# Kernel optimization log

Measured on AMD Instinct MI355X. Metric: run time of the kernel, lower is better.

## Reference

```python
import jax, jax.numpy as jnp
import numpy as np

K = 0.1            # manifold curvature param: points satisfy <x,x>_L = -1/K
H = 8              # num_heads
DH = 64            # head_spatial_dim
SP = 512           # spatial_dim = H*DH
SCALE = 1.0 / np.sqrt(DH)
SQRT_K = np.sqrt(K).astype(np.float32)


def _lorentz_fc(x, W, b):
    # Manifold-constrained FC: linear map to spatial coords, time recomputed
    sp = x @ W + b                                            # [..., out_spatial]
    t = jnp.sqrt(jnp.clip(1.0 / K + jnp.sum(sp * sp, axis=-1, keepdims=True), 1e-9, None))
    return jnp.concatenate([t, sp], axis=-1)


def _logmap0(p):
    # Lorentz log map at origin -> tangent spatial coords (time comp = 0)
    t, sp = p[..., :1], p[..., 1:]
    nrm = jnp.sqrt(jnp.sum(sp * sp, axis=-1, keepdims=True))
    theta = jnp.arccosh(jnp.clip(SQRT_K * t, 1.0 + 1e-7, None))
    return (theta / SQRT_K) * sp / jnp.maximum(nrm, 1e-9)


def _expmap0(u):
    nrm = jnp.sqrt(jnp.sum(u * u, axis=-1, keepdims=True))
    t = jnp.cosh(SQRT_K * nrm) / SQRT_K
    sp = jnp.sinh(SQRT_K * nrm) * u / (SQRT_K * jnp.maximum(nrm, 1e-9))
    return jnp.concatenate([t, sp], axis=-1)


def setup_inputs() -> dict:
    key = jax.random.key(0)
    ks = jax.random.split(key, 9)
    B, N = 4, 2048
    space = jax.random.normal(ks[0], (B, N, SP), dtype=jnp.float32) * 0.5
    t = jnp.sqrt(1.0 / K + jnp.sum(space * space, axis=-1, keepdims=True))
    x = jnp.concatenate([t, space], axis=-1)                  # on-manifold [B,N,513]
    s = (1 + SP) ** -0.5
    Wq = jax.random.normal(ks[1], (1 + SP, SP), dtype=jnp.float32) * s
    Wk = jax.random.normal(ks[2], (1 + SP, SP), dtype=jnp.float32) * s
    Wv = jax.random.normal(ks[3], (1 + SP, SP), dtype=jnp.float32) * s
    Wo = jax.random.normal(ks[4], (1 + SP, SP), dtype=jnp.float32) * s
    bq = jax.random.normal(ks[5], (SP,), dtype=jnp.float32) * 0.01
    bk = jax.random.normal(ks[6], (SP,), dtype=jnp.float32) * 0.01
    bv = jax.random.normal(ks[7], (SP,), dtype=jnp.float32) * 0.01
    bo = jax.random.normal(ks[8], (SP,), dtype=jnp.float32) * 0.01
    return {"x": x, "Wq": Wq, "bq": bq, "Wk": Wk, "bk": bk, "Wv": Wv, "bv": bv, "Wo": Wo, "bo": bo}


def _split_heads(p):
    # [B,N,1+H*DH] -> [B,H,N,1+DH], sharing the time component across heads
    B, N, _ = p.shape
    t = p[..., :1]                                            # [B,N,1]
    sp = p[..., 1:].reshape(B, N, H, DH)
    t = jnp.broadcast_to(t[:, :, None, :], (B, N, H, 1))
    return jnp.concatenate([t, sp], axis=-1).transpose(0, 2, 1, 3)


def reference(x, Wq, bq, Wk, bk, Wv, bv, Wo, bo):
    q = _split_heads(_lorentz_fc(x, Wq, bq))                  # [B,H,N,1+DH]
    k = _split_heads(_lorentz_fc(x, Wk, bk))
    v = _split_heads(_lorentz_fc(x, Wv, bv))
    # Lorentzian inner product scores: -q_t k_t + <q_s, k_s>
    scores = (jnp.einsum('bhnd,bhmd->bhnm', q[..., 1:], k[..., 1:])
              - jnp.einsum('bhni,bhmi->bhnm', q[..., :1], k[..., :1])) * SCALE
    attn = jax.nn.softmax(scores, axis=-1)                    # [B,H,N,N]
    # Riemannian aggregation: logmap0 -> weighted sum in tangent space -> expmap0
    v_tan = _logmap0(v)                                       # [B,H,N,DH]
    out_tan = jnp.einsum('bhnm,bhmd->bhnd', attn, v_tan)
    out = _expmap0(out_tan)                                   # [B,H,N,1+DH]
    # direct head concat: stack spatial parts, renormalize time onto manifold
    B, _, N, _ = out.shape
    space_cat = out[..., 1:].transpose(0, 2, 1, 3).reshape(B, N, H * DH)
    t_prime = jnp.sqrt(jnp.clip(1.0 / K + jnp.sum(space_cat * space_cat, axis=-1, keepdims=True), 1e-9, None))
    cat = jnp.concatenate([t_prime, space_cat], axis=-1)      # [B,N,513]
    return _lorentz_fc(cat, Wo, bo)                           # [B,N,513]
```

## Files before the change

### kernel.cpp

```cpp
#include <hip/hip_runtime.h>
#include <math.h>

#define H_    8
#define DH_   64
#define SPD   512
#define NSEQ  2048
#define BATCH 4
#define ROWS  8192
#define KDIM  513
#define INVK  10.0f
#define SQRTK 0.31622776601683794f
#define S2C   0.18033688011112043f
#define LOG2E 1.4426950408889634f
#define TKOFF 12.0f

using bf16x8 = __attribute__((ext_vector_type(8))) short;
using f32x4  = __attribute__((ext_vector_type(4))) float;
using f32x16 = __attribute__((ext_vector_type(16))) float;

static __device__ __forceinline__ short f2bf(float f){
  union { float f; unsigned u; } v; v.f = f;
  unsigned r = v.u + 0x7fffu + ((v.u >> 16) & 1u);
  return (short)(r >> 16);
}
static __device__ __forceinline__ float bf2f(short s){
  union { unsigned u; float f; } v; v.u = ((unsigned)(unsigned short)s) << 16;
  return v.f;
}
static __device__ __forceinline__ unsigned cvtpk(float lo, float hi){
  unsigned r; asm("v_cvt_pk_bf16_f32 %0, %1, %2" : "=v"(r) : "v"(lo), "v"(hi)); return r;
}
static __device__ __forceinline__ void plswapu(unsigned& a, unsigned& b){
  asm("v_permlane32_swap_b32 %0, %1" : "+v"(a), "+v"(b));
}
static __device__ __forceinline__ float exp2v(float x){
  float r; asm("v_exp_f32 %0, %1" : "=v"(r) : "v"(x)); return r;
}

#define GL16(gp, lp) __builtin_amdgcn_global_load_lds( \
    (const __attribute__((address_space(1))) void*)(gp), \
    (__attribute__((address_space(3))) void*)(lp), 16, 0, 0)

__global__ __launch_bounds__(256) void conv_kernel(const float* __restrict__ x,
                                                   const float* __restrict__ Wq,
                                                   const float* __restrict__ Wk,
                                                   const float* __restrict__ Wv,
                                                   const float* __restrict__ Wo,
                                                   short* __restrict__ xs,
                                                   short* __restrict__ WT){
  const int bid = blockIdx.x;
  if (bid < 8192){
    const int i2 = (bid * 256 + threadIdx.x) * 2;
    const int r = i2 >> 9, c = i2 & 511;
    const float a = x[(size_t)r * KDIM + 1 + c];
    const float b = x[(size_t)r * KDIM + 2 + c];
    const unsigned pk = (unsigned)(unsigned short)f2bf(a) |
                        ((unsigned)(unsigned short)f2bf(b) << 16);
    *(unsigned*)(xs + (size_t)r * SPD + c) = pk;
  } else {
    const int q = bid - 8192;
    const int wsel = q >> 10;
    const float* W = (wsel == 0) ? Wq : (wsel == 1) ? Wk : (wsel == 2) ? Wv : Wo;
    const int i = (q & 1023) * 256 + threadIdx.x;
    const int n = i >> 9, k = i & 511;
    WT[(size_t)wsel * SPD * SPD + i] = f2bf(W[(size_t)(k + 1) * SPD + n]);
  }
}

template<bool BF16OUT, int BM, bool TSQ, bool FUSESSQ>
__global__ __launch_bounds__(256) void gemm_kernel(
    const short* __restrict__ A, const short* __restrict__ WTbase,
    int sel0, int sel1, int sel2,
    const float* __restrict__ bias0, const float* __restrict__ bias1,
    const float* __restrict__ bias2,
    const float* __restrict__ W00, const float* __restrict__ W01,
    const float* __restrict__ W02,
    const float* __restrict__ tvec, long tstride,
    float* __restrict__ ssqout,
    void* __restrict__ C0, void* __restrict__ C1, void* __restrict__ C2,
    int ldc, int coff)
{
  constexpr int NREP = (BM == 128) ? 4 : 2;
  const int z = blockIdx.z;
  const int sel = (z == 0) ? sel0 : (z == 1) ? sel1 : sel2;
  const short* BT = WTbase + (size_t)sel * SPD * SPD;
  const float* bias = (z == 0) ? bias0 : (z == 1) ? bias1 : bias2;
  const float* W0 = (z == 0) ? W00 : (z == 1) ? W01 : W02;
  void* C = (z == 0) ? C0 : (z == 1) ? C1 : C2;

  __shared__ short As[BM * 32];
  __shared__ short Bs[128 * 32];

  const int tid  = threadIdx.x;
  const int lane = tid & 63;
  const int wave = tid >> 6;
  const int row0 = blockIdx.x * BM;
  const int col0 = blockIdx.y * 128;
  const int wr = (BM == 128) ? (wave >> 1) * 64 : 0;
  const int wc = (BM == 128) ? (wave & 1) * 64 : wave * 32;
  const int rA  = lane & 15;
  const int kg2 = (lane >> 4) * 16;
  const int g4  = lane >> 4;

  f32x4 acc[4][NREP] = {};

  for (int kt = 0; kt < SPD / 32; ++kt){
    __syncthreads();
    #pragma unroll
    for (int p = 0; p < BM / 64; ++p){
      const int idx = p * 256 + tid;
      const int r = idx >> 2, c4 = idx & 3;
      const int gc = (c4 ^ ((r >> 1) & 3)) * 8;
      GL16(A + (size_t)(row0 + r) * SPD + kt * 32 + gc, (char*)As + idx * 16);
    }
    #pragma unroll
    for (int p = 0; p < 2; ++p){
      const int idx = p * 256 + tid;
      const int r = idx >> 2, c4 = idx & 3;
      const int gc = (c4 ^ ((r >> 1) & 3)) * 8;
      GL16(BT + (size_t)(col0 + r) * SPD + kt * 32 + gc, (char*)Bs + idx * 16);
    }
    asm volatile("s_waitcnt vmcnt(0)" ::: "memory");
    __syncthreads();
    bf16x8 af[4], bfr[NREP];
    #pragma unroll
    for (int m = 0; m < 4; ++m){
      const int r = wr + m * 16 + rA;
      af[m] = *(const bf16x8*)((const char*)As + ((r * 64 + kg2) ^ (((r >> 1) & 3) << 4)));
    }
    #pragma unroll
    for (int n = 0; n < NREP; ++n){
      const int r = wc + n * 16 + rA;
      bfr[n] = *(const bf16x8*)((const char*)Bs + ((r * 64 + kg2) ^ (((r >> 1) & 3) << 4)));
    }
    #pragma unroll
    for (int m = 0; m < 4; ++m)
      #pragma unroll
      for (int n = 0; n < NREP; ++n)
        acc[m][n] = __builtin_amdgcn_mfma_f32_16x16x32_bf16(af[m], bfr[n], acc[m][n], 0, 0, 0);
  }

  float trow[4][4];
  #pragma unroll
  for (int m = 0; m < 4; ++m)
    #pragma unroll
    for (int j = 0; j < 4; ++j){
      const float raw = tvec[(size_t)(row0 + wr + m * 16 + g4 * 4 + j) * tstride];
      trow[m][j] = TSQ ? sqrtf(fmaxf(INVK + raw, 1e-9f)) : raw;
    }

  float rssq[4][4];
  #pragma unroll
  for (int m = 0; m < 4; ++m)
    #pragma unroll
    for (int j = 0; j < 4; ++j) rssq[m][j] = 0.f;

  #pragma unroll
  for (int m = 0; m < 4; ++m){
    const int row = row0 + wr + m * 16 + g4 * 4;
    #pragma unroll
    for (int n = 0; n < NREP; ++n){
      const int col = col0 + wc + n * 16 + rA;
      const float bv = bias[col];
      const float w0 = W0[col];
      #pragma unroll
      for (int j = 0; j < 4; ++j){
        const float v = acc[m][n][j] + trow[m][j] * w0 + bv;
        if (FUSESSQ) rssq[m][j] += v * v;
        if (BF16OUT) ((short*)C)[(size_t)(row + j) * SPD + col] = f2bf(v);
        else         ((float*)C)[(size_t)(row + j) * ldc + coff + col] = v;
      }
    }
  }
  if (FUSESSQ){
    #pragma unroll
    for (int m = 0; m < 4; ++m)
      #pragma unroll
      for (int j = 0; j < 4; ++j){
        float s = rssq[m][j];
        s += __shfl_xor(s, 1, 64);
        s += __shfl_xor(s, 2, 64);
        s += __shfl_xor(s, 4, 64);
        s += __shfl_xor(s, 8, 64);
        if (rA == 0) atomicAdd(&ssqout[row0 + wr + m * 16 + g4 * 4 + j], s);
      }
  }
}

__global__ __launch_bounds__(256) void postqkv_kernel(
    const short* __restrict__ qb, const short* __restrict__ kb,
    const short* __restrict__ vb, float* __restrict__ tq,
    unsigned* __restrict__ tkpk, short* __restrict__ vtT)
{
  const int tid = threadIdx.x;
  const int lane = tid & 63;
  const int wv = tid >> 6;
  const int row0 = blockIdx.x * 8 + wv * 2;
  const int b = blockIdx.x >> 8;

  #pragma unroll
  for (int i = 0; i < 2; ++i){
    const int row = row0 + i;
    const int n = row & (NSEQ - 1);
    {
      union { bf16x8 v; short e[8]; } u;
      u.v = *(const bf16x8*)(qb + (size_t)row * SPD + lane * 8);
      float s = 0.f;
      #pragma unroll
      for (int j = 0; j < 8; ++j){ const float f = bf2f(u.e[j]); s += f * f; }
      #pragma unroll
      for (int m = 1; m <= 32; m <<= 1) s += __shfl_xor(s, m, 64);
      if (lane == 0) tq[row] = sqrtf(INVK + s);
    }
    {
      union { bf16x8 v; short e[8]; } u;
      u.v = *(const bf16x8*)(kb + (size_t)row * SPD + lane * 8);
      float s = 0.f;
      #pragma unroll
      for (int j = 0; j < 8; ++j){ const float f = bf2f(u.e[j]); s += f * f; }
      #pragma unroll
      for (int m = 1; m <= 32; m <<= 1) s += __shfl_xor(s, m, 64);
      if (lane == 0){
        const float tkm = sqrtf(INVK + s) - TKOFF;
        const short bhi = f2bf(tkm);
        const short blo = f2bf(tkm - bf2f(bhi));
        tkpk[row] = (unsigned)(unsigned short)bhi | ((unsigned)(unsigned short)blo << 16);
      }
    }
    {
      union { bf16x8 v; short e[8]; } u;
      u.v = *(const bf16x8*)(vb + (size_t)row * SPD + lane * 8);
      float f[8]; float sh = 0.f;
      #pragma unroll
      for (int j = 0; j < 8; ++j){ f[j] = bf2f(u.e[j]); sh += f[j] * f[j]; }
      sh += __shfl_xor(sh, 1, 64);
      sh += __shfl_xor(sh, 2, 64);
      sh += __shfl_xor(sh, 4, 64);
      float tot = sh;
      tot += __shfl_xor(tot, 8, 64);
      tot += __shfl_xor(tot, 16, 64);
      tot += __shfl_xor(tot, 32, 64);
      const float tv = sqrtf(INVK + tot);
      const float av = fmaxf(SQRTK * tv, 1.0f + 1e-7f);
      const float theta = __logf(av + sqrtf(av * av - 1.0f));
      const float fac = theta * (1.0f / SQRTK);
      const float inv = fac / fmaxf(sqrtf(sh), 1e-9f);
      const int h = lane >> 3;
      const int d0 = (lane & 7) * 8;
      short* dst = vtT + ((size_t)((b * H_ + h) * DH_ + d0)) * NSEQ + n;
      #pragma unroll
      for (int j = 0; j < 8; ++j) dst[(size_t)j * NSEQ] = f2bf(inv * f[j]);
    }
  }
}

__global__ __launch_bounds__(256) void attn_kernel(
    const short* __restrict__ qb, const short* __restrict__ kb,
    const short* __restrict__ vtT, const float* __restrict__ tqg,
    const unsigned* __restrict__ tkpk, short* __restrict__ catb,
    float* __restrict__ tps)
{
  int bid = blockIdx.x;
  bid = (bid & 7) * 64 + (bid >> 3);
  const int qt = bid & 15;
  const int bh = bid >> 4;
  const int b = bh >> 3, h = bh & 7;
  const int q0 = qt * 128;
  const int tid = threadIdx.x;
  const int lane = tid & 63;
  const int w = tid >> 6;
  const int l31 = lane & 31;
  const int hi = lane >> 5;
  const int rsw = (l31 & 7) << 4;

  __shared__ short Ks[2][64 * 64];
  __shared__ short Vs[2][64 * 64];
  __shared__ float lred[4][32];
  __shared__ unsigned tks[NSEQ];

  const int qrow = q0 + w * 32 + l31;
  bf16x8 qf[4];
  {
    const short* qptr = qb + (size_t)(b * NSEQ + qrow) * SPD + h * DH_ + hi * 8;
    #pragma unroll
    for (int s = 0; s < 4; ++s){
      union { bf16x8 v; short e[8]; } u;
      u.v = *(const bf16x8*)(qptr + s * 16);
      #pragma unroll
      for (int j = 0; j < 8; ++j) u.e[j] = f2bf(bf2f(u.e[j]) * S2C);
      qf[s] = u.v;
    }
  }
  bf16x8 qf4;
  {
    const float a = -S2C * tqg[b * NSEQ + qrow];
    const short ahi = f2bf(a);
    const short alo = f2bf(a - bf2f(ahi));
    union { unsigned u[4]; bf16x8 v; } q4;
    q4.u[0] = hi ? 0u : ((unsigned)(unsigned short)ahi | ((unsigned)(unsigned short)alo << 16));
    q4.u[1] = hi ? 0u : (unsigned)(unsigned short)ahi;
    q4.u[2] = 0; q4.u[3] = 0;
    qf4 = q4.v;
  }
  bf16x8 onesB;
  {
    const unsigned val = (l31 == 0) ? 0x3f803f80u : 0u;
    union { unsigned u[4]; bf16x8 v; } ob;
    ob.u[0] = val; ob.u[1] = val; ob.u[2] = val; ob.u[3] = val;
    onesB = ob.v;
  }

  {
    const unsigned* tsrc = tkpk + b * NSEQ + tid * 8;
    *(uint4*)&tks[tid * 8]     = *(const uint4*)tsrc;
    *(uint4*)&tks[tid * 8 + 4] = *(const uint4*)(tsrc + 4);
  }

  int koff[2][4];
  #pragma unroll
  for (int f = 0; f < 2; ++f)
    #pragma unroll
    for (int s = 0; s < 4; ++s)
      koff[f][s] = (f * 32 + l31) * 128 + ((s * 32 + hi * 16) ^ rsw);

  const int rB = tid >> 3;
  const int c0 = (tid & 7) * 16;
  const int cc = c0 ^ ((rB & 7) << 4);
  const short* kbase = kb + (size_t)(b * NSEQ) * SPD + h * DH_;
  const short* vbase = vtT + (size_t)(bh * DH_) * NSEQ;

  uint4 kA0, kA1, vA0, vA1;
  uint4 kB0, kB1, vB0, vB1;

#define LOADA(m0) do{ \
    kA0 = *(const uint4*)(kbase + (size_t)((m0) + rB) * SPD + (c0 >> 1)); \
    kA1 = *(const uint4*)(kbase + (size_t)((m0) + 32 + rB) * SPD + (c0 >> 1)); \
    vA0 = *(const uint4*)(vbase + (size_t)rB * NSEQ + (m0) + (c0 >> 1)); \
    vA1 = *(const uint4*)(vbase + (size_t)(32 + rB) * NSEQ + (m0) + (c0 >> 1)); }while(0)
#define LOADB(m0) do{ \
    kB0 = *(const uint4*)(kbase + (size_t)((m0) + rB) * SPD + (c0 >> 1)); \
    kB1 = *(const uint4*)(kbase + (size_t)((m0) + 32 + rB) * SPD + (c0 >> 1)); \
    vB0 = *(const uint4*)(vbase + (size_t)rB * NSEQ + (m0) + (c0 >> 1)); \
    vB1 = *(const uint4*)(vbase + (size_t)(32 + rB) * NSEQ + (m0) + (c0 >> 1)); }while(0)
#define WRITEA(buf) do{ \
    *(uint4*)((char*)Ks[buf] + rB * 128 + cc) = kA0; \
    *(uint4*)((char*)Ks[buf] + (32 + rB) * 128 + cc) = kA1; \
    *(uint4*)((char*)Vs[buf] + rB * 128 + cc) = vA0; \
    *(uint4*)((char*)Vs[buf] + (32 + rB) * 128 + cc) = vA1; }while(0)
#define WRITEB(buf) do{ \
    *(uint4*)((char*)Ks[buf] + rB * 128 + cc) = kB0; \
    *(uint4*)((char*)Ks[buf] + (32 + rB) * 128 + cc) = kB1; \
    *(uint4*)((char*)Vs[buf] + rB * 128 + cc) = vB0; \
    *(uint4*)((char*)Vs[buf] + (32 + rB) * 128 + cc) = vB1; }while(0)
#define BARRIER() asm volatile("s_waitcnt lgkmcnt(0)\n\ts_barrier" ::: "memory")
#define WAITV4()  asm volatile("s_waitcnt vmcnt(4)" ::: "memory")
#define WAITV0()  asm volatile("s_waitcnt vmcnt(0)" ::: "memory")

  f32x16 o[2] = {};
  f32x16 lacc = {};
  const f32x16 z16 = {};

  auto KAUG = [&](unsigned pk)->bf16x8{
    union { unsigned u[4]; bf16x8 v; } ka;
    ka.u[0] = hi ? 0u : ((pk & 0xFFFFu) | (pk << 16));
    ka.u[1] = hi ? 0u : (pk >> 16);
    ka.u[2] = 0; ka.u[3] = 0;
    return ka.v;
  };

  auto COMPUTE = [&](const char* Kc, const char* Vc, int m0){
    const unsigned pk0 = tks[m0 + l31];
    const unsigned pk1 = tks[m0 + 32 + l31];

    f32x16 sacc[2];
    __builtin_amdgcn_s_setprio(1);
    #pragma unroll
    for (int f = 0; f < 2; ++f){
      {
        const bf16x8 kf = *(const bf16x8*)(Kc + koff[f][0]);
        sacc[f] = __builtin_amdgcn_mfma_f32_32x32x16_bf16(kf, qf[0], z16, 0, 0, 0);
      }
      #pragma unroll
      for (int s = 1; s < 4; ++s){
        const bf16x8 kf = *(const bf16x8*)(Kc + koff[f][s]);
        sacc[f] = __builtin_amdgcn_mfma_f32_32x32x16_bf16(kf, qf[s], sacc[f], 0, 0, 0);
      }
    }
    sacc[0] = __builtin_amdgcn_mfma_f32_32x32x16_bf16(KAUG(pk0), qf4, sacc[0], 0, 0, 0);
    sacc[1] = __builtin_amdgcn_mfma_f32_32x32x16_bf16(KAUG(pk1), qf4, sacc[1], 0, 0, 0);
    __builtin_amdgcn_s_setprio(0);

    #pragma unroll
    for (int f = 0; f < 2; ++f)
      #pragma unroll
      for (int e = 0; e < 16; ++e)
        sacc[f][e] = exp2v(sacc[f][e]);

    bf16x8 pa[4];
    #pragma unroll
    for (int f = 0; f < 2; ++f)
      #pragma unroll
      for (int g16 = 0; g16 < 2; ++g16){
        const int bse = g16 * 8;
        unsigned A0 = cvtpk(sacc[f][bse + 0], sacc[f][bse + 1]);
        unsigned A1 = cvtpk(sacc[f][bse + 2], sacc[f][bse + 3]);
        unsigned B0 = cvtpk(sacc[f][bse + 4], sacc[f][bse + 5]);
        unsigned B1 = cvtpk(sacc[f][bse + 6], sacc[f][bse + 7]);
        plswapu(A0, B0);
        plswapu(A1, B1);
        union { unsigned u[4]; bf16x8 v; } pu;
        pu.u[0] = A0; pu.u[1] = A1; pu.u[2] = B0; pu.u[3] = B1;
        pa[f * 2 + g16] = pu.v;
      }

    __builtin_amdgcn_s_setprio(1);
    #pragma unroll
    for (int db = 0; db < 2; ++db)
      #pragma unroll
      for (int ks = 0; ks < 4; ++ks){
        const bf16x8 vf = *(const bf16x8*)(Vc + koff[db][ks]);
        o[db] = __builtin_amdgcn_mfma_f32_32x32x16_bf16(pa[ks], vf, o[db], 0, 0, 0);
      }
    #pragma unroll
    for (int ks = 0; ks < 4; ++ks)
      lacc = __builtin_amdgcn_mfma_f32_32x32x16_bf16(pa[ks], onesB, lacc, 0, 0, 0);
    __builtin_amdgcn_s_setprio(0);
  };

  LOADA(0);
  WAITV0();
  WRITEA(0);
  __syncthreads();
  LOADB(64);

  const int NT = NSEQ / 64;
  #pragma unroll 1
  for (int t = 0; t < NT; t += 2){
    const int m0 = t * 64;
    if (t + 2 < NT) LOADA(m0 + 128);
    COMPUTE((const char*)Ks[0], (const char*)Vs[0], m0);
    if (t + 2 < NT) WAITV4(); else WAITV0();
    WRITEB(1);
    BARRIER();
    if (t + 3 < NT) LOADB(m0 + 192);
    COMPUTE((const char*)Ks[1], (const char*)Vs[1], m0 + 64);
    if (t + 2 < NT){
      if (t + 3 < NT) WAITV4(); else WAITV0();
      WRITEA(0);
    }
    BARRIER();
  }

  if (l31 == 0){
    #pragma unroll
    for (int e = 0; e < 16; ++e)
      lred[w][(e & 3) + 8 * (e >> 2) + 4 * hi] = lacc[e];
  }
  asm volatile("s_waitcnt lgkmcnt(0)" ::: "memory");
  f32x4 lv[4];
  #pragma unroll
  for (int g = 0; g < 4; ++g) lv[g] = *(const f32x4*)&lred[w][8 * g + 4 * hi];

  const int brow = b * NSEQ + q0 + w * 32;
  const size_t obase = (size_t)brow * SPD + h * DH_ + l31;
  #pragma unroll
  for (int e = 0; e < 16; ++e){
    const float linv = __builtin_amdgcn_rcpf(lv[e >> 2][e & 3]);
    const float ov0 = o[0][e] * linv;
    const float ov1 = o[1][e] * linv;
    float ss = ov0 * ov0 + ov1 * ov1;
    #pragma unroll
    for (int off = 16; off; off >>= 1) ss += __shfl_xor(ss, off, 64);
    const float nrm = sqrtf(ss);
    const float e2 = exp2f(SQRTK * nrm * LOG2E);
    const float einv = __builtin_amdgcn_rcpf(e2);
    const float fac = (e2 - einv) * 0.5f * __builtin_amdgcn_rcpf(SQRTK * fmaxf(nrm, 1e-9f));
    const int crow = (e & 3) + 8 * (e >> 2) + 4 * hi;
    catb[obase + (size_t)crow * SPD]      = f2bf(fac * ov0);
    catb[obase + (size_t)crow * SPD + 32] = f2bf(fac * ov1);
    if (l31 == 0) atomicAdd(&tps[brow + crow], fac * fac * ss);
  }
#undef LOADA
#undef LOADB
#undef WRITEA
#undef WRITEB
#undef BARRIER
#undef WAITV4
#undef WAITV0
}

__global__ __launch_bounds__(256) void fin2_kernel(float* __restrict__ out,
                                                   const float* __restrict__ tos){
  const int r = blockIdx.x * 256 + threadIdx.x;
  out[(size_t)r * KDIM] = sqrtf(fmaxf(INVK + tos[r], 1e-9f));
}

extern "C" void kernel_launch(void* const* d_in, const int* in_sizes, int n_in,
                              void* d_out, int out_size, void* d_ws, size_t ws_size,
                              hipStream_t stream)
{
  (void)in_sizes; (void)n_in; (void)out_size; (void)ws_size;
  const float* x  = (const float*)d_in[0];
  const float* Wq = (const float*)d_in[1];
  const float* bq = (const float*)d_in[2];
  const float* Wk = (const float*)d_in[3];
  const float* bk = (const float*)d_in[4];
  const float* Wv = (const float*)d_in[5];
  const float* bv = (const float*)d_in[6];
  const float* Wo = (const float*)d_in[7];
  const float* bo = (const float*)d_in[8];
  float* out = (float*)d_out;

  char* p = (char*)d_ws;
  short* xs   = (short*)p; p += (size_t)ROWS * SPD * 2;
  short* WT   = (short*)p; p += (size_t)4 * SPD * SPD * 2;
  short* qb   = (short*)p; p += (size_t)ROWS * SPD * 2;
  short* kb   = (short*)p; p += (size_t)ROWS * SPD * 2;
  short* vb   = (short*)p; p += (size_t)ROWS * SPD * 2;
  short* vtT  = (short*)p; p += (size_t)ROWS * SPD * 2;
  float* tq   = (float*)p; p += (size_t)ROWS * 4;
  unsigned* tkpk = (unsigned*)p; p += (size_t)ROWS * 4;
  short* catb = (short*)p; p += (size_t)ROWS * SPD * 2;
  float* tps  = (float*)p; p += (size_t)ROWS * 4;
  float* tos  = (float*)p; p += (size_t)ROWS * 4;

  hipMemsetAsync(tps, 0, (size_t)2 * ROWS * 4, stream);
  conv_kernel<<<8192 + 4096, 256, 0, stream>>>(x, Wq, Wk, Wv, Wo, xs, WT);
  gemm_kernel<true, 128, false, false><<<dim3(64, 4, 3), 256, 0, stream>>>(
      xs, WT, 0, 1, 2, bq, bk, bv, Wq, Wk, Wv, x, (long)KDIM, nullptr,
      qb, kb, vb, SPD, 0);
  postqkv_kernel<<<1024, 256, 0, stream>>>(qb, kb, vb, tq, tkpk, vtT);
  attn_kernel<<<512, 256, 0, stream>>>(qb, kb, vtT, tq, tkpk, catb, tps);
  gemm_kernel<false, 64, true, true><<<dim3(128, 4, 1), 256, 0, stream>>>(
      catb, WT, 3, 3, 3, bo, bo, bo, Wo, Wo, Wo, tps, 1L, tos,
      out, out, out, KDIM, 1);
  fin2_kernel<<<ROWS / 256, 256, 0, stream>>>(out, tos);
}
```

Measured before the change: 149.0 us.

## Double attention key tile to 128 and move time-norm sum to separate kernel

The attention kernel now processes 128 keys per pipeline stage instead of 64, so each K/V LDS buffer doubles and half as many barriers and loop iterations are needed. The per-row atomic accumulation of the head-concat time component is removed from attention and replaced by a small tp_kernel that recomputes the squared norm from the bf16 cat buffer. The aim is less synchronisation overhead and no atomics, at the cost of more LDS and registers per block, which may lower occupancy. The recomputation also adds an extra launch and a read of catb, and it uses bf16-rounded values instead of fp32 ones.

```diff
diff --git a/kernel.cpp b/kernel.cpp
--- a/kernel.cpp
+++ b/kernel.cpp
@@ -67,7 +67,7 @@
   }
 }
 
-template<bool BF16OUT, int BM, bool TSQ, bool FUSESSQ>
+template<bool BF16OUT, int BM, bool FUSESSQ>
 __global__ __launch_bounds__(256) void gemm_kernel(
     const short* __restrict__ A, const short* __restrict__ WTbase,
     int sel0, int sel1, int sel2,
@@ -144,10 +144,8 @@
   #pragma unroll
   for (int m = 0; m < 4; ++m)
     #pragma unroll
-    for (int j = 0; j < 4; ++j){
-      const float raw = tvec[(size_t)(row0 + wr + m * 16 + g4 * 4 + j) * tstride];
-      trow[m][j] = TSQ ? sqrtf(fmaxf(INVK + raw, 1e-9f)) : raw;
-    }
+    for (int j = 0; j < 4; ++j)
+      trow[m][j] = tvec[(size_t)(row0 + wr + m * 16 + g4 * 4 + j) * tstride];
 
   float rssq[4][4];
   #pragma unroll
@@ -257,8 +255,7 @@
 __global__ __launch_bounds__(256) void attn_kernel(
     const short* __restrict__ qb, const short* __restrict__ kb,
     const short* __restrict__ vtT, const float* __restrict__ tqg,
-    const unsigned* __restrict__ tkpk, short* __restrict__ catb,
-    float* __restrict__ tps)
+    const unsigned* __restrict__ tkpk, short* __restrict__ catb)
 {
   int bid = blockIdx.x;
   bid = (bid & 7) * 64 + (bid >> 3);
@@ -271,10 +268,9 @@
   const int w = tid >> 6;
   const int l31 = lane & 31;
   const int hi = lane >> 5;
-  const int rsw = (l31 & 7) << 4;
-
-  __shared__ short Ks[2][64 * 64];
-  __shared__ short Vs[2][64 * 64];
+
+  __shared__ short Ks[2][128 * 64];
+  __shared__ short Vs[2][64 * 128];
   __shared__ float lred[4][32];
   __shared__ unsigned tks[NSEQ];
 
@@ -316,44 +312,44 @@
     *(uint4*)&tks[tid * 8 + 4] = *(const uint4*)(tsrc + 4);
   }
 
-  int koff[2][4];
-  #pragma unroll
-  for (int f = 0; f < 2; ++f)
+  int koffK[4][4];
+  #pragma unroll
+  for (int f = 0; f < 4; ++f)
     #pragma unroll
     for (int s = 0; s < 4; ++s)
-      koff[f][s] = (f * 32 + l31) * 128 + ((s * 32 + hi * 16) ^ rsw);
-
-  const int rB = tid >> 3;
-  const int c0 = (tid & 7) * 16;
-  const int cc = c0 ^ ((rB & 7) << 4);
+      koffK[f][s] = (f * 32 + l31) * 128 + ((s * 32 + hi * 16) ^ ((l31 & 7) << 4));
+  int koffV[2][8];
+  #pragma unroll
+  for (int db = 0; db < 2; ++db)
+    #pragma unroll
+    for (int ks = 0; ks < 8; ++ks)
+      koffV[db][ks] = (db * 32 + l31) * 256 + ((ks * 32 + hi * 16) ^ ((l31 & 15) << 4));
+
+  const int rK = tid >> 3;
+  const int cK = (tid & 7) * 16;
+  const int ccK = cK ^ ((rK & 7) << 4);
+  const int rV = tid >> 4;
+  const int cV = (tid & 15) * 16;
+  const int ccV = cV ^ ((rV & 15) << 4);
   const short* kbase = kb + (size_t)(b * NSEQ) * SPD + h * DH_;
   const short* vbase = vtT + (size_t)(bh * DH_) * NSEQ;
 
-  uint4 kA0, kA1, vA0, vA1;
-  uint4 kB0, kB1, vB0, vB1;
-
-#define LOADA(m0) do{ \
-    kA0 = *(const uint4*)(kbase + (size_t)((m0) + rB) * SPD + (c0 >> 1)); \
-    kA1 = *(const uint4*)(kbase + (size_t)((m0) + 32 + rB) * SPD + (c0 >> 1)); \
-    vA0 = *(const uint4*)(vbase + (size_t)rB * NSEQ + (m0) + (c0 >> 1)); \
-    vA1 = *(const uint4*)(vbase + (size_t)(32 + rB) * NSEQ + (m0) + (c0 >> 1)); }while(0)
-#define LOADB(m0) do{ \
-    kB0 = *(const uint4*)(kbase + (size_t)((m0) + rB) * SPD + (c0 >> 1)); \
-    kB1 = *(const uint4*)(kbase + (size_t)((m0) + 32 + rB) * SPD + (c0 >> 1)); \
-    vB0 = *(const uint4*)(vbase + (size_t)rB * NSEQ + (m0) + (c0 >> 1)); \
-    vB1 = *(const uint4*)(vbase + (size_t)(32 + rB) * NSEQ + (m0) + (c0 >> 1)); }while(0)
-#define WRITEA(buf) do{ \
-    *(uint4*)((char*)Ks[buf] + rB * 128 + cc) = kA0; \
-    *(uint4*)((char*)Ks[buf] + (32 + rB) * 128 + cc) = kA1; \
-    *(uint4*)((char*)Vs[buf] + rB * 128 + cc) = vA0; \
-    *(uint4*)((char*)Vs[buf] + (32 + rB) * 128 + cc) = vA1; }while(0)
-#define WRITEB(buf) do{ \
-    *(uint4*)((char*)Ks[buf] + rB * 128 + cc) = kB0; \
-    *(uint4*)((char*)Ks[buf] + (32 + rB) * 128 + cc) = kB1; \
-    *(uint4*)((char*)Vs[buf] + rB * 128 + cc) = vB0; \
-    *(uint4*)((char*)Vs[buf] + (32 + rB) * 128 + cc) = vB1; }while(0)
+  uint4 kA[4], vA[4], kB[4], vB[4];
+
+#define LOADA(m0) do{ _Pragma("unroll") for (int g = 0; g < 4; ++g){ \
+    kA[g] = *(const uint4*)(kbase + (size_t)((m0) + g * 32 + rK) * SPD + (cK >> 1)); \
+    vA[g] = *(const uint4*)(vbase + (size_t)(g * 16 + rV) * NSEQ + (m0) + (cV >> 1)); } }while(0)
+#define LOADB(m0) do{ _Pragma("unroll") for (int g = 0; g < 4; ++g){ \
+    kB[g] = *(const uint4*)(kbase + (size_t)((m0) + g * 32 + rK) * SPD + (cK >> 1)); \
+    vB[g] = *(const uint4*)(vbase + (size_t)(g * 16 + rV) * NSEQ + (m0) + (cV >> 1)); } }while(0)
+#define WRITEA(buf) do{ _Pragma("unroll") for (int g = 0; g < 4; ++g){ \
+    *(uint4*)((char*)Ks[buf] + (g * 32 + rK) * 128 + ccK) = kA[g]; \
+    *(uint4*)((char*)Vs[buf] + (g * 16 + rV) * 256 + ccV) = vA[g]; } }while(0)
+#define WRITEB(buf) do{ _Pragma("unroll") for (int g = 0; g < 4; ++g){ \
+    *(uint4*)((char*)Ks[buf] + (g * 32 + rK) * 128 + ccK) = kB[g]; \
+    *(uint4*)((char*)Vs[buf] + (g * 16 + rV) * 256 + ccV) = vB[g]; } }while(0)
 #define BARRIER() asm volatile("s_waitcnt lgkmcnt(0)\n\ts_barrier" ::: "memory")
-#define WAITV4()  asm volatile("s_waitcnt vmcnt(4)" ::: "memory")
+#define WAITV8()  asm volatile("s_waitcnt vmcnt(8)" ::: "memory")
 #define WAITV0()  asm volatile("s_waitcnt vmcnt(0)" ::: "memory")
 
   f32x16 o[2] = {};
@@ -369,36 +365,36 @@
   };
 
   auto COMPUTE = [&](const char* Kc, const char* Vc, int m0){
-    const unsigned pk0 = tks[m0 + l31];
-    const unsigned pk1 = tks[m0 + 32 + l31];
-
-    f32x16 sacc[2];
+    unsigned pk[4];
+    #pragma unroll
+    for (int f = 0; f < 4; ++f) pk[f] = tks[m0 + f * 32 + l31];
+
+    f32x16 sacc[4];
     __builtin_amdgcn_s_setprio(1);
     #pragma unroll
-    for (int f = 0; f < 2; ++f){
+    for (int f = 0; f < 4; ++f){
       {
-        const bf16x8 kf = *(const bf16x8*)(Kc + koff[f][0]);
+        const bf16x8 kf = *(const bf16x8*)(Kc + koffK[f][0]);
         sacc[f] = __builtin_amdgcn_mfma_f32_32x32x16_bf16(kf, qf[0], z16, 0, 0, 0);
       }
       #pragma unroll
       for (int s = 1; s < 4; ++s){
-        const bf16x8 kf = *(const bf16x8*)(Kc + koff[f][s]);
+        const bf16x8 kf = *(const bf16x8*)(Kc + koffK[f][s]);
         sacc[f] = __builtin_amdgcn_mfma_f32_32x32x16_bf16(kf, qf[s], sacc[f], 0, 0, 0);
       }
-    }
-    sacc[0] = __builtin_amdgcn_mfma_f32_32x32x16_bf16(KAUG(pk0), qf4, sacc[0], 0, 0, 0);
-    sacc[1] = __builtin_amdgcn_mfma_f32_32x32x16_bf16(KAUG(pk1), qf4, sacc[1], 0, 0, 0);
+      sacc[f] = __builtin_amdgcn_mfma_f32_32x32x16_bf16(KAUG(pk[f]), qf4, sacc[f], 0, 0, 0);
+    }
     __builtin_amdgcn_s_setprio(0);
 
     #pragma unroll
-    for (int f = 0; f < 2; ++f)
+    for (int f = 0; f < 4; ++f)
       #pragma unroll
       for (int e = 0; e < 16; ++e)
         sacc[f][e] = exp2v(sacc[f][e]);
 
-    bf16x8 pa[4];
-    #pragma unroll
-    for (int f = 0; f < 2; ++f)
+    bf16x8 pa[8];
+    #pragma unroll
+    for (int f = 0; f < 4; ++f)
       #pragma unroll
       for (int g16 = 0; g16 < 2; ++g16){
         const int bse = g16 * 8;
@@ -417,12 +413,12 @@
     #pragma unroll
     for (int db = 0; db < 2; ++db)
       #pragma unroll
-      for (int ks = 0; ks < 4; ++ks){
-        const bf16x8 vf = *(const bf16x8*)(Vc + koff[db][ks]);
+      for (int ks = 0; ks < 8; ++ks){
+        const bf16x8 vf = *(const bf16x8*)(Vc + koffV[db][ks]);
         o[db] = __builtin_amdgcn_mfma_f32_32x32x16_bf16(pa[ks], vf, o[db], 0, 0, 0);
       }
     #pragma unroll
-    for (int ks = 0; ks < 4; ++ks)
+    for (int ks = 0; ks < 8; ++ks)
       lacc = __builtin_amdgcn_mfma_f32_32x32x16_bf16(pa[ks], onesB, lacc, 0, 0, 0);
     __builtin_amdgcn_s_setprio(0);
   };
@@ -431,21 +427,21 @@
   WAITV0();
   WRITEA(0);
   __syncthreads();
-  LOADB(64);
-
-  const int NT = NSEQ / 64;
+  LOADB(128);
+
+  const int NT = NSEQ / 128;
   #pragma unroll 1
   for (int t = 0; t < NT; t += 2){
-    const int m0 = t * 64;
-    if (t + 2 < NT) LOADA(m0 + 128);
+    const int m0 = t * 128;
+    if (t + 2 < NT) LOADA(m0 + 256);
     COMPUTE((const char*)Ks[0], (const char*)Vs[0], m0);
-    if (t + 2 < NT) WAITV4(); else WAITV0();
+    if (t + 2 < NT) WAITV8(); else WAITV0();
     WRITEB(1);
     BARRIER();
-    if (t + 3 < NT) LOADB(m0 + 192);
-    COMPUTE((const char*)Ks[1], (const char*)Vs[1], m0 + 64);
+    if (t + 3 < NT) LOADB(m0 + 384);
+    COMPUTE((const char*)Ks[1], (const char*)Vs[1], m0 + 128);
     if (t + 2 < NT){
-      if (t + 3 < NT) WAITV4(); else WAITV0();
+      if (t + 3 < NT) WAITV8(); else WAITV0();
       WRITEA(0);
     }
     BARRIER();
@@ -461,8 +457,7 @@
   #pragma unroll
   for (int g = 0; g < 4; ++g) lv[g] = *(const f32x4*)&lred[w][8 * g + 4 * hi];
 
-  const int brow = b * NSEQ + q0 + w * 32;
-  const size_t obase = (size_t)brow * SPD + h * DH_ + l31;
+  const size_t obase = (size_t)(b * NSEQ + q0 + w * 32) * SPD + h * DH_ + l31;
   #pragma unroll
   for (int e = 0; e < 16; ++e){
     const float linv = __builtin_amdgcn_rcpf(lv[e >> 2][e & 3]);
@@ -478,15 +473,28 @@
     const int crow = (e & 3) + 8 * (e >> 2) + 4 * hi;
     catb[obase + (size_t)crow * SPD]      = f2bf(fac * ov0);
     catb[obase + (size_t)crow * SPD + 32] = f2bf(fac * ov1);
-    if (l31 == 0) atomicAdd(&tps[brow + crow], fac * fac * ss);
   }
 #undef LOADA
 #undef LOADB
 #undef WRITEA
 #undef WRITEB
 #undef BARRIER
-#undef WAITV4
+#undef WAITV8
 #undef WAITV0
+}
+
+__global__ __launch_bounds__(256) void tp_kernel(const short* __restrict__ catb,
+                                                 float* __restrict__ tps){
+  const int lane = threadIdx.x & 63;
+  const int row = blockIdx.x * 4 + (threadIdx.x >> 6);
+  union { bf16x8 v; short e[8]; } u;
+  u.v = *(const bf16x8*)(catb + (size_t)row * SPD + lane * 8);
+  float s = 0.f;
+  #pragma unroll
+  for (int j = 0; j < 8; ++j){ const float f = bf2f(u.e[j]); s += f * f; }
+  #pragma unroll
+  for (int m = 1; m <= 32; m <<= 1) s += __shfl_xor(s, m, 64);
+  if (lane == 0) tps[row] = sqrtf(fmaxf(INVK + s, 1e-9f));
 }
 
 __global__ __launch_bounds__(256) void fin2_kernel(float* __restrict__ out,
@@ -524,14 +532,15 @@
   float* tps  = (float*)p; p += (size_t)ROWS * 4;
   float* tos  = (float*)p; p += (size_t)ROWS * 4;
 
-  hipMemsetAsync(tps, 0, (size_t)2 * ROWS * 4, stream);
+  hipMemsetAsync(tos, 0, (size_t)ROWS * 4, stream);
   conv_kernel<<<8192 + 4096, 256, 0, stream>>>(x, Wq, Wk, Wv, Wo, xs, WT);
-  gemm_kernel<true, 128, false, false><<<dim3(64, 4, 3), 256, 0, stream>>>(
+  gemm_kernel<true, 128, false><<<dim3(64, 4, 3), 256, 0, stream>>>(
       xs, WT, 0, 1, 2, bq, bk, bv, Wq, Wk, Wv, x, (long)KDIM, nullptr,
       qb, kb, vb, SPD, 0);
   postqkv_kernel<<<1024, 256, 0, stream>>>(qb, kb, vb, tq, tkpk, vtT);
-  attn_kernel<<<512, 256, 0, stream>>>(qb, kb, vtT, tq, tkpk, catb, tps);
-  gemm_kernel<false, 64, true, true><<<dim3(128, 4, 1), 256, 0, stream>>>(
+  attn_kernel<<<512, 256, 0, stream>>>(qb, kb, vtT, tq, tkpk, catb);
+  tp_kernel<<<ROWS / 4, 256, 0, stream>>>(catb, tps);
+  gemm_kernel<false, 64, true><<<dim3(128, 4, 1), 256, 0, stream>>>(
       catb, WT, 3, 3, 3, bo, bo, bo, Wo, Wo, Wo, tps, 1L, tos,
       out, out, out, KDIM, 1);
   fin2_kernel<<<ROWS / 256, 256, 0, stream>>>(out, tos);
```

Measured after the change: 212.6 us. 42.7% more time.
